# Kernel optimization log

Hardware: AMD Instinct MI355X
Metric: run time of the kernel (lower is better)

Reference implementation:

```python
import jax, jax.numpy as jnp
import numpy as np

N, E, FN, FE, L, G = 4096, 16384, 16, 8, 128, 64
EPS = 1e-5


def setup_inputs() -> dict:
    key = jax.random.key(0)
    ks = iter(jax.random.split(key, 40))

    def lin_w(shape):
        return jax.random.normal(next(ks), shape, jnp.float32) * (1.0 / np.sqrt(shape[0]))

    d = {}
    d["x"] = jax.random.normal(next(ks), (N, FN), jnp.float32)
    d["edge_attr"] = jax.random.normal(next(ks), (E, FE), jnp.float32)
    d["edge_index"] = jax.random.randint(next(ks), (2, E), 0, N)
    d["batch"] = jnp.sort(jax.random.randint(next(ks), (N,), 0, G))
    for i, (cin, cout) in enumerate([(FN, 32), (32, 64), (64, 128)], 1):
        d[f"We{i}"] = lin_w((FE, cin * cout))          # edge_fc weight
        d[f"be{i}"] = jnp.zeros((cin * cout,), jnp.float32)
        d[f"bias{i}"] = jnp.zeros((cout,), jnp.float32)
        d[f"Wr{i}"] = lin_w((cin, cout))               # res_fc weight
        d[f"br{i}"] = jnp.zeros((cout,), jnp.float32)
        d[f"bn_g{i}"] = jnp.ones((cout,), jnp.float32)
        d[f"bn_b{i}"] = jnp.zeros((cout,), jnp.float32)
        d[f"a{i}"] = jnp.float32(0.25)                  # PReLU slope
    d["Wi"] = lin_w((128, 128)); d["bi"] = jnp.zeros((128,), jnp.float32)
    d["Wj"] = lin_w((128, 128)); d["bj"] = jnp.zeros((128,), jnp.float32)
    d["Wfc"] = lin_w((128, 2 * L)); d["bfc"] = jnp.zeros((2 * L,), jnp.float32)
    return d


def _ecc(x, src, dst, norm, edge_attr, We, be, bias, Wr, br, cout, cin):
    # dynamically generated per-edge filter: [E, out, in]
    theta = (edge_attr @ We + be).reshape(E, cout, cin)
    # gather source features, per-edge matvec, degree-normalize (norm_j)
    msg = norm[src][:, None] * jnp.einsum('eoi,ei->eo', theta, x[src])
    # scatter-add into destination nodes + bias + residual linear
    return jax.ops.segment_sum(msg, dst, num_segments=N) + bias + x @ Wr + br


def _bn(x, g, b):
    m = x.mean(0)
    v = x.var(0)  # biased variance, as torch BN training normalization
    return (x - m) * jax.lax.rsqrt(v + EPS) * g + b


def _prelu(x, a):
    return jnp.where(x >= 0, x, a * x)


def reference(x, edge_attr, edge_index, batch,
              We1, be1, bias1, Wr1, br1, bn_g1, bn_b1, a1,
              We2, be2, bias2, Wr2, br2, bn_g2, bn_b2, a2,
              We3, be3, bias3, Wr3, br3, bn_g3, bn_b3, a3,
              Wi, bi, Wj, bj, Wfc, bfc):
    src, dst = edge_index[0], edge_index[1]
    deg = jax.ops.segment_sum(jnp.ones((E,), x.dtype), src, num_segments=N)
    norm = jnp.where(deg > 0, 1.0 / deg, 0.0)

    h = _ecc(x, src, dst, norm, edge_attr, We1, be1, bias1, Wr1, br1, 32, FN)
    h = _prelu(_bn(h, bn_g1, bn_b1), a1)
    h = _ecc(h, src, dst, norm, edge_attr, We2, be2, bias2, Wr2, br2, 64, 32)
    h = _prelu(_bn(h, bn_g2, bn_b2), a2)
    h = _ecc(h, src, dst, norm, edge_attr, We3, be3, bias3, Wr3, br3, 128, 64)
    h = _prelu(_bn(h, bn_g3, bn_b3), a3)

    # gated attention pooling (GGS-NN eq. 7), scatter-sum per graph
    gates = jax.nn.sigmoid(h @ Wi + bi)
    feats = jnp.tanh(h @ Wj + bj)
    pooled = jnp.tanh(jax.ops.segment_sum(gates * feats, batch, num_segments=G))

    z = pooled @ Wfc + bfc  # [G, 2L]
    return z[:, :L], z[:, L:]
```

## Files before the change

kernel.cpp:

```cpp
#include <hip/hip_runtime.h>
#include <math.h>

#define NN 4096
#define NE 16384
#define NG 64

#define OFF_DEG   0
#define OFF_ST1   4096
#define OFF_ST2   4160
#define OFF_ST3   4288
#define OFF_POOL  4544
#define ZERO_FLOATS 12736
#define OFF_H1    12736
#define OFF_H2    143808
#define OFF_H3    405952
#define OFF_WX1   930240
#define OFF_WX2   935360
#define OFF_WX3   955840
#define OFF_Y     1037760

__device__ __forceinline__ void build_wext(const float* We, const float* be,
                                           const float* Wr, float* Wx,
                                           int CIN, int C, int t) {
    int NC = 10 * C;
    int i = t / NC; int col = t - i * NC;
    float v;
    if (col < 8 * C)      { int f = col / C, o = col - f * C; v = We[f * CIN * C + o * CIN + i]; }
    else if (col < 9 * C) { int o = col - 8 * C;              v = be[o * CIN + i]; }
    else                  { int o = col - 9 * C;              v = Wr[i * C + o]; }
    Wx[t] = v;
}

__global__ __launch_bounds__(256) void k_prep(
    const float* __restrict__ We1, const float* __restrict__ be1, const float* __restrict__ Wr1,
    const float* __restrict__ We2, const float* __restrict__ be2, const float* __restrict__ Wr2,
    const float* __restrict__ We3, const float* __restrict__ be3, const float* __restrict__ Wr3,
    const int* __restrict__ ei, float* __restrict__ ws)
{
    int t = blockIdx.x * 256 + threadIdx.x;
    if (t < 5120)  { build_wext(We1, be1, Wr1, ws + OFF_WX1, 16, 32, t); return; }
    t -= 5120;
    if (t < 20480) { build_wext(We2, be2, Wr2, ws + OFF_WX2, 32, 64, t); return; }
    t -= 20480;
    if (t < 81920) { build_wext(We3, be3, Wr3, ws + OFF_WX3, 64, 128, t); return; }
    t -= 81920;
    if (t < NE)    { atomicAdd(&ws[OFF_DEG + ei[t]], 1.0f); }
}

template<int K, int C, bool BN>
__global__ __launch_bounds__(256) void k_proj(
    const float* __restrict__ A, const float* __restrict__ Bw,
    const float* __restrict__ st, const float* __restrict__ bg,
    const float* __restrict__ bb, const float* __restrict__ alpha,
    const float* __restrict__ bias, const float* __restrict__ br,
    float* __restrict__ Y, float* __restrict__ h)
{
    constexpr int NC = 10 * C;
    __shared__ float sA[K][68];
    __shared__ float sB[K][68];
    __shared__ float sS[K], sT[K];
    const int tid = threadIdx.x;
    const int m0 = blockIdx.x * 64;
    const int n0 = blockIdx.y * 64;

    float al = 0.f;
    if constexpr (BN) {
        if (tid < K) {
            float mean = st[tid] * (1.f / NN);
            float var  = st[K + tid] * (1.f / NN) - mean * mean;
            var = fmaxf(var, 0.f);
            float s = rsqrtf(var + 1e-5f) * bg[tid];
            sS[tid] = s; sT[tid] = bb[tid] - mean * s;
        }
        al = alpha[0];
        __syncthreads();
    }
    for (int t = tid; t < 64 * K; t += 256) {
        int m = t / K, i = t - m * K;
        float v = A[(m0 + m) * K + i];
        if constexpr (BN) { v = sS[i] * v + sT[i]; v = v >= 0.f ? v : al * v; }
        sA[i][m] = v;
    }
    for (int t = tid; t < 64 * K; t += 256) {
        int i = t / 64, n = t - i * 64;
        sB[i][n] = Bw[i * NC + n0 + n];
    }
    __syncthreads();

    const int tn = tid % 16, tm = tid / 16;
    float acc[4][4] = {{0.f}};
#pragma unroll 8
    for (int i = 0; i < K; ++i) {
        float4 a = *(const float4*)&sA[i][tm * 4];
        float4 b = *(const float4*)&sB[i][tn * 4];
        acc[0][0] += a.x * b.x; acc[0][1] += a.x * b.y; acc[0][2] += a.x * b.z; acc[0][3] += a.x * b.w;
        acc[1][0] += a.y * b.x; acc[1][1] += a.y * b.y; acc[1][2] += a.y * b.z; acc[1][3] += a.y * b.w;
        acc[2][0] += a.z * b.x; acc[2][1] += a.z * b.y; acc[2][2] += a.z * b.z; acc[2][3] += a.z * b.w;
        acc[3][0] += a.w * b.x; acc[3][1] += a.w * b.y; acc[3][2] += a.w * b.z; acc[3][3] += a.w * b.w;
    }

    if (n0 + 64 <= 9 * C) {
#pragma unroll
        for (int mm = 0; mm < 4; ++mm) {
            int m = m0 + tm * 4 + mm;
            float4 v = make_float4(acc[mm][0], acc[mm][1], acc[mm][2], acc[mm][3]);
            *(float4*)&Y[(size_t)m * (9 * C) + n0 + tn * 4] = v;
        }
    } else if (n0 >= 9 * C) {
        int o = n0 - 9 * C + tn * 4;
        float4 add = *(const float4*)&bias[o];
        float4 ad2 = *(const float4*)&br[o];
#pragma unroll
        for (int mm = 0; mm < 4; ++mm) {
            int m = m0 + tm * 4 + mm;
            float4 v = make_float4(acc[mm][0] + add.x + ad2.x, acc[mm][1] + add.y + ad2.y,
                                   acc[mm][2] + add.z + ad2.z, acc[mm][3] + add.w + ad2.w);
            *(float4*)&h[(size_t)m * C + o] = v;
        }
    } else {
#pragma unroll
        for (int mm = 0; mm < 4; ++mm) {
            int m = m0 + tm * 4 + mm;
#pragma unroll
            for (int nn = 0; nn < 4; ++nn) {
                int col = n0 + tn * 4 + nn;
                if (col < 9 * C) Y[(size_t)m * (9 * C) + col] = acc[mm][nn];
                else { int o = col - 9 * C; h[(size_t)m * C + o] = acc[mm][nn] + bias[o] + br[o]; }
            }
        }
    }
}

template<int C>
__global__ __launch_bounds__(256) void k_egather(
    const float* __restrict__ Y, const float* __restrict__ eattr,
    const int* __restrict__ ei, const float* __restrict__ deg,
    float* __restrict__ h)
{
    constexpr int Q = C / 4;
    int idx = blockIdx.x * 256 + threadIdx.x;
    int e = idx / Q;
    int q = idx - e * Q;
    int src = ei[e], dst = ei[NE + e];
    float d = deg[src];
    float nrm = d > 0.f ? 1.f / d : 0.f;
    const float4* y = (const float4*)(Y + (size_t)src * (9 * C));
    const float* ea = eattr + e * 8;
    float4 acc = y[8 * Q + q];
#pragma unroll
    for (int f = 0; f < 8; ++f) {
        float4 yf = y[f * Q + q];
        float w = ea[f];
        acc.x += w * yf.x; acc.y += w * yf.y; acc.z += w * yf.z; acc.w += w * yf.w;
    }
    float* hp = h + (size_t)dst * C + q * 4;
    atomicAdd(hp + 0, acc.x * nrm);
    atomicAdd(hp + 1, acc.y * nrm);
    atomicAdd(hp + 2, acc.z * nrm);
    atomicAdd(hp + 3, acc.w * nrm);
}

template<int C>
__global__ __launch_bounds__(256) void k_bnstat(const float* __restrict__ h, float* __restrict__ st)
{
    constexpr int NL = 256 / C;
    __shared__ float sred[256];
    const int tid = threadIdx.x;
    const int o = tid % C, nl = tid / C;
    const int rbase = blockIdx.x * 64;
    float sum = 0.f, sq = 0.f;
    for (int r = nl; r < 64; r += NL) {
        float v = h[(size_t)(rbase + r) * C + o];
        sum += v; sq += v * v;
    }
    sred[tid] = sum;
    __syncthreads();
    if (tid < C) {
        float s = 0.f;
        for (int g2 = 0; g2 < NL; ++g2) s += sred[g2 * C + tid];
        atomicAdd(&st[tid], s);
    }
    __syncthreads();
    sred[tid] = sq;
    __syncthreads();
    if (tid < C) {
        float s = 0.f;
        for (int g2 = 0; g2 < NL; ++g2) s += sred[g2 * C + tid];
        atomicAdd(&st[C + tid], s);
    }
}

__global__ __launch_bounds__(256) void k_pool(
    const float* __restrict__ h3, const int* __restrict__ batch,
    const float* __restrict__ st, const float* __restrict__ bg,
    const float* __restrict__ bb, const float* __restrict__ alpha,
    const float* __restrict__ Wi, const float* __restrict__ bi,
    const float* __restrict__ Wj, const float* __restrict__ bj,
    float* __restrict__ pooled)
{
    constexpr int KN = 8, NB = 16;
    __shared__ float sH[NB * 128];
    __shared__ float sS[128], sT[128];
    __shared__ int sB[NB];
    const int tid = threadIdx.x;
    const int nbase = blockIdx.x * NB;
    if (tid < 128) {
        float mean = st[tid] * (1.f / NN);
        float var  = st[128 + tid] * (1.f / NN) - mean * mean;
        var = fmaxf(var, 0.f);
        float s = rsqrtf(var + 1e-5f) * bg[tid];
        sS[tid] = s; sT[tid] = bb[tid] - mean * s;
    }
    float al = alpha[0];
    __syncthreads();
    for (int t = tid; t < NB * 128; t += 256) {
        int i = t % 128;
        float v = sS[i] * h3[(size_t)nbase * 128 + t] + sT[i];
        sH[t] = v >= 0.f ? v : al * v;
    }
    if (tid < NB) sB[tid] = batch[nbase + tid];
    __syncthreads();

    const int o = tid % 128, nl = tid / 128;
    float gacc[KN], facc[KN];
#pragma unroll
    for (int k = 0; k < KN; ++k) { gacc[k] = 0.f; facc[k] = 0.f; }
    for (int i = 0; i < 128; ++i) {
        float wi = Wi[i * 128 + o], wj = Wj[i * 128 + o];
#pragma unroll
        for (int k = 0; k < KN; ++k) {
            float hv = sH[(nl * KN + k) * 128 + i];
            gacc[k] += hv * wi;
            facc[k] += hv * wj;
        }
    }
    float bio = bi[o], bjo = bj[o];
#pragma unroll
    for (int k = 0; k < KN; ++k) {
        int r = nl * KN + k;
        float gate = 1.f / (1.f + expf(-(gacc[k] + bio)));
        float feat = tanhf(facc[k] + bjo);
        atomicAdd(&pooled[sB[r] * 128 + o], gate * feat);
    }
}

__global__ __launch_bounds__(256) void k_final(
    const float* __restrict__ pooled, const float* __restrict__ Wfc,
    const float* __restrict__ bfc, float* __restrict__ out)
{
    __shared__ float sP[128];
    const int g = blockIdx.x, c = threadIdx.x;
    if (c < 128) sP[c] = tanhf(pooled[g * 128 + c]);
    __syncthreads();
    float z = bfc[c];
    for (int i = 0; i < 128; ++i) z += sP[i] * Wfc[i * 256 + c];
    int oidx = (c < 128) ? (g * 128 + c) : (NG * 128 + g * 128 + (c - 128));
    out[oidx] = z;
}

extern "C" void kernel_launch(void* const* d_in, const int* in_sizes, int n_in,
                              void* d_out, int out_size, void* d_ws, size_t ws_size,
                              hipStream_t stream)
{
    (void)in_sizes; (void)n_in; (void)out_size; (void)ws_size;
    const float* x     = (const float*)d_in[0];
    const float* eattr = (const float*)d_in[1];
    const int*   ei    = (const int*)d_in[2];
    const int*   batch = (const int*)d_in[3];
    const float* We1 = (const float*)d_in[4];
    const float* be1 = (const float*)d_in[5];
    const float* bias1 = (const float*)d_in[6];
    const float* Wr1 = (const float*)d_in[7];
    const float* br1 = (const float*)d_in[8];
    const float* bg1 = (const float*)d_in[9];
    const float* bb1 = (const float*)d_in[10];
    const float* a1  = (const float*)d_in[11];
    const float* We2 = (const float*)d_in[12];
    const float* be2 = (const float*)d_in[13];
    const float* bias2 = (const float*)d_in[14];
    const float* Wr2 = (const float*)d_in[15];
    const float* br2 = (const float*)d_in[16];
    const float* bg2 = (const float*)d_in[17];
    const float* bb2 = (const float*)d_in[18];
    const float* a2  = (const float*)d_in[19];
    const float* We3 = (const float*)d_in[20];
    const float* be3 = (const float*)d_in[21];
    const float* bias3 = (const float*)d_in[22];
    const float* Wr3 = (const float*)d_in[23];
    const float* br3 = (const float*)d_in[24];
    const float* bg3 = (const float*)d_in[25];
    const float* bb3 = (const float*)d_in[26];
    const float* a3  = (const float*)d_in[27];
    const float* Wi  = (const float*)d_in[28];
    const float* bi  = (const float*)d_in[29];
    const float* Wj  = (const float*)d_in[30];
    const float* bj  = (const float*)d_in[31];
    const float* Wfc = (const float*)d_in[32];
    const float* bfc = (const float*)d_in[33];
    float* ws  = (float*)d_ws;
    float* out = (float*)d_out;

    hipMemsetAsync(d_ws, 0, (size_t)ZERO_FLOATS * sizeof(float), stream);
    k_prep<<<484, 256, 0, stream>>>(We1, be1, Wr1, We2, be2, Wr2, We3, be3, Wr3, ei, ws);

    k_proj<16, 32, false><<<dim3(64, 5), 256, 0, stream>>>(
        x, ws + OFF_WX1, nullptr, nullptr, nullptr, nullptr, bias1, br1, ws + OFF_Y, ws + OFF_H1);
    k_egather<32><<<NE * 8 / 256, 256, 0, stream>>>(ws + OFF_Y, eattr, ei, ws + OFF_DEG, ws + OFF_H1);
    k_bnstat<32><<<64, 256, 0, stream>>>(ws + OFF_H1, ws + OFF_ST1);

    k_proj<32, 64, true><<<dim3(64, 10), 256, 0, stream>>>(
        ws + OFF_H1, ws + OFF_WX2, ws + OFF_ST1, bg1, bb1, a1, bias2, br2, ws + OFF_Y, ws + OFF_H2);
    k_egather<64><<<NE * 16 / 256, 256, 0, stream>>>(ws + OFF_Y, eattr, ei, ws + OFF_DEG, ws + OFF_H2);
    k_bnstat<64><<<64, 256, 0, stream>>>(ws + OFF_H2, ws + OFF_ST2);

    k_proj<64, 128, true><<<dim3(64, 20), 256, 0, stream>>>(
        ws + OFF_H2, ws + OFF_WX3, ws + OFF_ST2, bg2, bb2, a2, bias3, br3, ws + OFF_Y, ws + OFF_H3);
    k_egather<128><<<NE * 32 / 256, 256, 0, stream>>>(ws + OFF_Y, eattr, ei, ws + OFF_DEG, ws + OFF_H3);
    k_bnstat<128><<<64, 256, 0, stream>>>(ws + OFF_H3, ws + OFF_ST3);

    k_pool<<<NN / 16, 256, 0, stream>>>(ws + OFF_H3, batch, ws + OFF_ST3, bg3, bb3, a3,
                                        Wi, bi, Wj, bj, ws + OFF_POOL);
    k_final<<<NG, 256, 0, stream>>>(ws + OFF_POOL, Wfc, bfc, out);
}
```

Baseline: 274.4 us.

## Replace atomic edge scatter with CSR dst-gather fused with BN stats; fuse pooling

Builds a destination-sorted CSR edge list (degree counts in prep, a single-block scan and fill kernel) so each node gathers its incoming edge messages instead of scattering with float atomics. The gather kernel also accumulates the batch-norm sums, so the separate stats kernels are dropped. Pooling and the final linear layer are merged into one per-graph kernel that finds each graph's node range by binary search, removing the pooled atomics and a launch. Costs include a serial single-block CSR build, per-channel scalar loads in the gather, and only 64 blocks doing the pooling work.

```diff
diff --git a/kernel.cpp b/kernel.cpp
--- a/kernel.cpp
+++ b/kernel.cpp
@@ -6,18 +6,20 @@
 #define NG 64
 
 #define OFF_DEG   0
-#define OFF_ST1   4096
-#define OFF_ST2   4160
-#define OFF_ST3   4288
-#define OFF_POOL  4544
-#define ZERO_FLOATS 12736
-#define OFF_H1    12736
-#define OFF_H2    143808
-#define OFF_H3    405952
-#define OFF_WX1   930240
-#define OFF_WX2   935360
-#define OFF_WX3   955840
-#define OFF_Y     1037760
+#define OFF_DCNT  4096
+#define OFF_ST1   8192
+#define OFF_ST2   8256
+#define OFF_ST3   8384
+#define ZERO_FLOATS 8640
+#define OFF_OFFS  8704
+#define OFF_LIST  12864
+#define OFF_H1    29248
+#define OFF_H2    160320
+#define OFF_H3    422464
+#define OFF_WX1   946752
+#define OFF_WX2   951872
+#define OFF_WX3   972352
+#define OFF_Y     1054272
 
 __device__ __forceinline__ void build_wext(const float* We, const float* be,
                                            const float* Wr, float* Wx,
@@ -44,7 +46,37 @@
     t -= 20480;
     if (t < 81920) { build_wext(We3, be3, Wr3, ws + OFF_WX3, 64, 128, t); return; }
     t -= 81920;
-    if (t < NE)    { atomicAdd(&ws[OFF_DEG + ei[t]], 1.0f); }
+    if (t < NE)    { atomicAdd(&ws[OFF_DEG + ei[t]], 1.0f); return; }
+    t -= NE;
+    if (t < NE)    { atomicAdd((int*)ws + OFF_DCNT + ei[NE + t], 1); }
+}
+
+__global__ __launch_bounds__(256) void k_csr(const int* __restrict__ ei, float* __restrict__ ws)
+{
+    __shared__ int cur[NN];
+    __shared__ int part[256];
+    int* dcnt = (int*)ws + OFF_DCNT;
+    int* offs = (int*)ws + OFF_OFFS;
+    int* list = (int*)ws + OFF_LIST;
+    const int tid = threadIdx.x;
+    const int base = tid * 16;
+    int tmp[16]; int s = 0;
+#pragma unroll
+    for (int k = 0; k < 16; ++k) { tmp[k] = dcnt[base + k]; s += tmp[k]; }
+    part[tid] = s;
+    __syncthreads();
+    if (tid == 0) { int run = 0; for (int i = 0; i < 256; ++i) { int v = part[i]; part[i] = run; run += v; } }
+    __syncthreads();
+    int run = part[tid];
+#pragma unroll
+    for (int k = 0; k < 16; ++k) { cur[base + k] = run; offs[base + k] = run; run += tmp[k]; }
+    if (tid == 255) offs[NN] = run;
+    __syncthreads();
+    for (int e = tid; e < NE; e += 256) {
+        int d = ei[NE + e];
+        int pos = atomicAdd(&cur[d], 1);
+        list[pos] = e;
+    }
 }
 
 template<int K, int C, bool BN>
@@ -132,52 +164,41 @@
 }
 
 template<int C>
-__global__ __launch_bounds__(256) void k_egather(
+__global__ __launch_bounds__(256) void k_enode(
     const float* __restrict__ Y, const float* __restrict__ eattr,
     const int* __restrict__ ei, const float* __restrict__ deg,
-    float* __restrict__ h)
-{
-    constexpr int Q = C / 4;
-    int idx = blockIdx.x * 256 + threadIdx.x;
-    int e = idx / Q;
-    int q = idx - e * Q;
-    int src = ei[e], dst = ei[NE + e];
-    float d = deg[src];
-    float nrm = d > 0.f ? 1.f / d : 0.f;
-    const float4* y = (const float4*)(Y + (size_t)src * (9 * C));
-    const float* ea = eattr + e * 8;
-    float4 acc = y[8 * Q + q];
-#pragma unroll
-    for (int f = 0; f < 8; ++f) {
-        float4 yf = y[f * Q + q];
-        float w = ea[f];
-        acc.x += w * yf.x; acc.y += w * yf.y; acc.z += w * yf.z; acc.w += w * yf.w;
-    }
-    float* hp = h + (size_t)dst * C + q * 4;
-    atomicAdd(hp + 0, acc.x * nrm);
-    atomicAdd(hp + 1, acc.y * nrm);
-    atomicAdd(hp + 2, acc.z * nrm);
-    atomicAdd(hp + 3, acc.w * nrm);
-}
-
-template<int C>
-__global__ __launch_bounds__(256) void k_bnstat(const float* __restrict__ h, float* __restrict__ st)
+    const int* __restrict__ offs, const int* __restrict__ list,
+    float* __restrict__ h, float* __restrict__ st)
 {
     constexpr int NL = 256 / C;
     __shared__ float sred[256];
     const int tid = threadIdx.x;
     const int o = tid % C, nl = tid / C;
-    const int rbase = blockIdx.x * 64;
+    const int n0 = blockIdx.x * 16;
     float sum = 0.f, sq = 0.f;
-    for (int r = nl; r < 64; r += NL) {
-        float v = h[(size_t)(rbase + r) * C + o];
-        sum += v; sq += v * v;
+    for (int r = nl; r < 16; r += NL) {
+        const int n = n0 + r;
+        const int e0 = offs[n], e1 = offs[n + 1];
+        float acc = h[(size_t)n * C + o];
+        for (int e = e0; e < e1; ++e) {
+            const int eid = list[e];
+            const int src = ei[eid];
+            const float nrm = 1.f / deg[src];
+            const float* y = Y + (size_t)src * (9 * C);
+            const float* ea = eattr + eid * 8;
+            float a = y[8 * C + o];
+#pragma unroll
+            for (int f = 0; f < 8; ++f) a += ea[f] * y[f * C + o];
+            acc += a * nrm;
+        }
+        h[(size_t)n * C + o] = acc;
+        sum += acc; sq += acc * acc;
     }
     sred[tid] = sum;
     __syncthreads();
     if (tid < C) {
         float s = 0.f;
-        for (int g2 = 0; g2 < NL; ++g2) s += sred[g2 * C + tid];
+        for (int l = 0; l < NL; ++l) s += sred[l * C + tid];
         atomicAdd(&st[tid], s);
     }
     __syncthreads();
@@ -185,25 +206,25 @@
     __syncthreads();
     if (tid < C) {
         float s = 0.f;
-        for (int g2 = 0; g2 < NL; ++g2) s += sred[g2 * C + tid];
+        for (int l = 0; l < NL; ++l) s += sred[l * C + tid];
         atomicAdd(&st[C + tid], s);
     }
 }
 
-__global__ __launch_bounds__(256) void k_pool(
+__global__ __launch_bounds__(256) void k_poolfinal(
     const float* __restrict__ h3, const int* __restrict__ batch,
     const float* __restrict__ st, const float* __restrict__ bg,
     const float* __restrict__ bb, const float* __restrict__ alpha,
     const float* __restrict__ Wi, const float* __restrict__ bi,
     const float* __restrict__ Wj, const float* __restrict__ bj,
-    float* __restrict__ pooled)
-{
-    constexpr int KN = 8, NB = 16;
-    __shared__ float sH[NB * 128];
+    const float* __restrict__ Wfc, const float* __restrict__ bfc,
+    float* __restrict__ out)
+{
     __shared__ float sS[128], sT[128];
-    __shared__ int sB[NB];
-    const int tid = threadIdx.x;
-    const int nbase = blockIdx.x * NB;
+    __shared__ float sH[8][128];
+    __shared__ float sG[8][128];
+    __shared__ float sP[128];
+    const int g = blockIdx.x, tid = threadIdx.x;
     if (tid < 128) {
         float mean = st[tid] * (1.f / NN);
         float var  = st[128 + tid] * (1.f / NN) - mean * mean;
@@ -211,50 +232,46 @@
         float s = rsqrtf(var + 1e-5f) * bg[tid];
         sS[tid] = s; sT[tid] = bb[tid] - mean * s;
     }
-    float al = alpha[0];
-    __syncthreads();
-    for (int t = tid; t < NB * 128; t += 256) {
-        int i = t % 128;
-        float v = sS[i] * h3[(size_t)nbase * 128 + t] + sT[i];
-        sH[t] = v >= 0.f ? v : al * v;
-    }
-    if (tid < NB) sB[tid] = batch[nbase + tid];
-    __syncthreads();
-
-    const int o = tid % 128, nl = tid / 128;
-    float gacc[KN], facc[KN];
-#pragma unroll
-    for (int k = 0; k < KN; ++k) { gacc[k] = 0.f; facc[k] = 0.f; }
-    for (int i = 0; i < 128; ++i) {
-        float wi = Wi[i * 128 + o], wj = Wj[i * 128 + o];
-#pragma unroll
-        for (int k = 0; k < KN; ++k) {
-            float hv = sH[(nl * KN + k) * 128 + i];
-            gacc[k] += hv * wi;
-            facc[k] += hv * wj;
-        }
-    }
-    float bio = bi[o], bjo = bj[o];
-#pragma unroll
-    for (int k = 0; k < KN; ++k) {
-        int r = nl * KN + k;
-        float gate = 1.f / (1.f + expf(-(gacc[k] + bio)));
-        float feat = tanhf(facc[k] + bjo);
-        atomicAdd(&pooled[sB[r] * 128 + o], gate * feat);
-    }
-}
-
-__global__ __launch_bounds__(256) void k_final(
-    const float* __restrict__ pooled, const float* __restrict__ Wfc,
-    const float* __restrict__ bfc, float* __restrict__ out)
-{
-    __shared__ float sP[128];
-    const int g = blockIdx.x, c = threadIdx.x;
-    if (c < 128) sP[c] = tanhf(pooled[g * 128 + c]);
-    __syncthreads();
-    float z = bfc[c];
-    for (int i = 0; i < 128; ++i) z += sP[i] * Wfc[i * 256 + c];
-    int oidx = (c < 128) ? (g * 128 + c) : (NG * 128 + g * 128 + (c - 128));
+    const float al = alpha[0];
+    int a = 0, b = NN;
+    while (a < b) { int m = (a + b) >> 1; if (batch[m] < g) a = m + 1; else b = m; }
+    const int ns = a;
+    a = 0; b = NN;
+    while (a < b) { int m = (a + b) >> 1; if (batch[m] <= g) a = m + 1; else b = m; }
+    const int ne = a;
+    __syncthreads();
+
+    const int o = tid & 127, w = tid >> 7;
+    const float* Wg = w ? Wj : Wi;
+    const float bo = w ? bj[o] : bi[o];
+    float accP = 0.f;
+    for (int c0 = ns; c0 < ne; c0 += 8) {
+        const int cs = min(8, ne - c0);
+        __syncthreads();
+        for (int u = tid; u < cs * 128; u += 256) {
+            int k = u >> 7, i = u & 127;
+            float v = sS[i] * h3[(size_t)(c0 + k) * 128 + i] + sT[i];
+            sH[k][i] = v >= 0.f ? v : al * v;
+        }
+        __syncthreads();
+        float d[8];
+#pragma unroll
+        for (int k = 0; k < 8; ++k) d[k] = 0.f;
+        for (int i = 0; i < 128; ++i) {
+            float wv = Wg[i * 128 + o];
+#pragma unroll
+            for (int k = 0; k < 8; ++k) d[k] += sH[k][i] * wv;
+        }
+        if (w == 0) for (int k = 0; k < cs; ++k) sG[k][o] = 1.f / (1.f + expf(-(d[k] + bo)));
+        __syncthreads();
+        if (w == 1) for (int k = 0; k < cs; ++k) accP += sG[k][o] * tanhf(d[k] + bo);
+    }
+    __syncthreads();
+    if (w == 1) sP[o] = tanhf(accP);
+    __syncthreads();
+    float z = bfc[tid];
+    for (int i = 0; i < 128; ++i) z += sP[i] * Wfc[i * 256 + tid];
+    const int oidx = (tid < 128) ? g * 128 + tid : NG * 128 + g * 128 + (tid - 128);
     out[oidx] = z;
 }
 
@@ -299,26 +316,25 @@
     const float* bfc = (const float*)d_in[33];
     float* ws  = (float*)d_ws;
     float* out = (float*)d_out;
+    const int* offs = (const int*)ws + OFF_OFFS;
+    const int* list = (const int*)ws + OFF_LIST;
 
     hipMemsetAsync(d_ws, 0, (size_t)ZERO_FLOATS * sizeof(float), stream);
-    k_prep<<<484, 256, 0, stream>>>(We1, be1, Wr1, We2, be2, Wr2, We3, be3, Wr3, ei, ws);
+    k_prep<<<548, 256, 0, stream>>>(We1, be1, Wr1, We2, be2, Wr2, We3, be3, Wr3, ei, ws);
+    k_csr<<<1, 256, 0, stream>>>(ei, ws);
 
     k_proj<16, 32, false><<<dim3(64, 5), 256, 0, stream>>>(
         x, ws + OFF_WX1, nullptr, nullptr, nullptr, nullptr, bias1, br1, ws + OFF_Y, ws + OFF_H1);
-    k_egather<32><<<NE * 8 / 256, 256, 0, stream>>>(ws + OFF_Y, eattr, ei, ws + OFF_DEG, ws + OFF_H1);
-    k_bnstat<32><<<64, 256, 0, stream>>>(ws + OFF_H1, ws + OFF_ST1);
-
+    k_enode<32><<<NN / 16, 256, 0, stream>>>(ws + OFF_Y, eattr, ei, ws + OFF_DEG, offs, list,
+                                             ws + OFF_H1, ws + OFF_ST1);
     k_proj<32, 64, true><<<dim3(64, 10), 256, 0, stream>>>(
         ws + OFF_H1, ws + OFF_WX2, ws + OFF_ST1, bg1, bb1, a1, bias2, br2, ws + OFF_Y, ws + OFF_H2);
-    k_egather<64><<<NE * 16 / 256, 256, 0, stream>>>(ws + OFF_Y, eattr, ei, ws + OFF_DEG, ws + OFF_H2);
-    k_bnstat<64><<<64, 256, 0, stream>>>(ws + OFF_H2, ws + OFF_ST2);
-
+    k_enode<64><<<NN / 16, 256, 0, stream>>>(ws + OFF_Y, eattr, ei, ws + OFF_DEG, offs, list,
+                                             ws + OFF_H2, ws + OFF_ST2);
     k_proj<64, 128, true><<<dim3(64, 20), 256, 0, stream>>>(
         ws + OFF_H2, ws + OFF_WX3, ws + OFF_ST2, bg2, bb2, a2, bias3, br3, ws + OFF_Y, ws + OFF_H3);
-    k_egather<128><<<NE * 32 / 256, 256, 0, stream>>>(ws + OFF_Y, eattr, ei, ws + OFF_DEG, ws + OFF_H3);
-    k_bnstat<128><<<64, 256, 0, stream>>>(ws + OFF_H3, ws + OFF_ST3);
-
-    k_pool<<<NN / 16, 256, 0, stream>>>(ws + OFF_H3, batch, ws + OFF_ST3, bg3, bb3, a3,
-                                        Wi, bi, Wj, bj, ws + OFF_POOL);
-    k_final<<<NG, 256, 0, stream>>>(ws + OFF_POOL, Wfc, bfc, out);
-}
+    k_enode<128><<<NN / 16, 256, 0, stream>>>(ws + OFF_Y, eattr, ei, ws + OFF_DEG, offs, list,
+                                              ws + OFF_H3, ws + OFF_ST3);
+    k_poolfinal<<<NG, 256, 0, stream>>>(ws + OFF_H3, batch, ws + OFF_ST3, bg3, bb3, a3,
+                                        Wi, bi, Wj, bj, Wfc, bfc, out);
+}
```

New measurement: 371.8 us. 1.35x slower.
